# Performance work log

Hardware: AMD Instinct MI355X
Metric: run time of the kernel (lower is better)

## Reference

```python
import jax, jax.numpy as jnp
import numpy as np

B, S, D, H = 4, 2048, 1024, 16
HD = D // H
THETA = 10000.0


def _rope(x, pos, theta):
    # x: (B, H, S, HD); rotate adjacent even/odd pairs
    half = x.shape[-1] // 2
    inv_freq = theta ** (-jnp.arange(half, dtype=x.dtype) / half)  # theta^(-2k/d)
    ang = pos[:, None].astype(x.dtype) * inv_freq[None, :]         # (S, half)
    cos, sin = jnp.cos(ang), jnp.sin(ang)
    x1, x2 = x[..., 0::2], x[..., 1::2]
    o1 = x1 * cos - x2 * sin
    o2 = x1 * sin + x2 * cos
    return jnp.stack([o1, o2], axis=-1).reshape(x.shape)


def setup_inputs() -> dict:
    key = jax.random.key(0)
    ks = jax.random.split(key, 5)
    sc = 1.0 / np.sqrt(D)
    return {
        "x": jax.random.normal(ks[0], (B, S, D), jnp.float32),
        "W_Q": jax.random.normal(ks[1], (D, D), jnp.float32) * sc,
        "W_K": jax.random.normal(ks[2], (D, D), jnp.float32) * sc,
        "W_V": jax.random.normal(ks[3], (D, D), jnp.float32) * sc,
        "W_O": jax.random.normal(ks[4], (D, D), jnp.float32) * sc,
    }


def reference(x, W_Q, W_K, W_V, W_O):
    b, s, d = x.shape
    split = lambda t: t.reshape(b, s, H, HD).transpose(0, 2, 1, 3)  # (B,H,S,HD)
    q = split(x @ W_Q.T)
    k = split(x @ W_K.T)
    v = split(x @ W_V.T)
    pos = jnp.arange(s)
    q = _rope(q, pos, THETA)
    k = _rope(k, pos, THETA)
    scale = 1.0 / jnp.sqrt(jnp.asarray(HD, x.dtype))
    scores = jnp.einsum("bhqd,bhkd->bhqk", q, k) * scale
    causal = jnp.tril(jnp.ones((s, s), dtype=bool))
    scores = jnp.where(causal, scores, jnp.asarray(-jnp.inf, x.dtype))
    attn = jax.nn.softmax(scores, axis=-1)
    o = jnp.einsum("bhqk,bhkd->bhqd", attn, v)
    o = o.transpose(0, 2, 1, 3).reshape(b, s, d)
    return o @ W_O.T
```

## Files before the change

### kernel.cpp

```cpp
#include <hip/hip_runtime.h>
#include <hip/hip_bf16.h>
#include <stdint.h>

#define B_ 4
#define S_ 2048
#define D_ 1024
#define H_ 16

typedef __attribute__((ext_vector_type(4))) float f32x4;
typedef __attribute__((ext_vector_type(16))) float f32x16;
typedef __attribute__((ext_vector_type(8))) short short8;
typedef __attribute__((ext_vector_type(8))) unsigned short ushort8;
typedef __attribute__((ext_vector_type(4))) unsigned int u32x4;
typedef unsigned short u16;
typedef unsigned int u32;

__device__ __forceinline__ u16 f2bf(float f){
  return __builtin_bit_cast(u16, __hip_bfloat16(f));
}
__device__ __forceinline__ u32 pk2bf(float a, float b){
  return (u32)f2bf(a) | ((u32)f2bf(b) << 16);
}
__device__ __forceinline__ float rexp2(float x){
  float r; asm("v_exp_f32 %0, %1" : "=v"(r) : "v"(x)); return r;
}
__device__ __forceinline__ u32 cvtpk(float a, float b){
  u32 r; asm("v_cvt_pk_bf16_f32 %0, %1, %2" : "=v"(r) : "v"(a), "v"(b)); return r;
}
__device__ __forceinline__ f32x4 mfma16(short8 a, short8 b, f32x4 c){
  return __builtin_amdgcn_mfma_f32_16x16x32_bf16(a, b, c, 0, 0, 0);
}
__device__ __forceinline__ f32x16 mfma32(short8 a, short8 b, f32x16 c){
  return __builtin_amdgcn_mfma_f32_32x32x16_bf16(a, b, c, 0, 0, 0);
}
__device__ __forceinline__ void plswap(u32 &x, u32 &y){
  asm volatile("v_permlane32_swap_b32 %0, %1" : "+v"(x), "+v"(y));
}
__device__ __forceinline__ void gload16(const u16* g, u16* l){
  __builtin_amdgcn_global_load_lds((const __attribute__((address_space(1))) u32*)g,
                                   (__attribute__((address_space(3))) u32*)l, 16, 0, 0);
}

__global__ __launch_bounds__(256) void prep_kernel(const float* __restrict__ x,
                                                   const float* __restrict__ w0, const float* __restrict__ w1,
                                                   const float* __restrict__ w2, const float* __restrict__ w3,
                                                   u16* __restrict__ xb,
                                                   u16* __restrict__ o0, u16* __restrict__ o1,
                                                   u16* __restrict__ o2, u16* __restrict__ o3,
                                                   float2* __restrict__ tab){
  const int gid = blockIdx.x;
  if (gid < 8192){
    const int i = gid * 256 + threadIdx.x;
    float4 v = reinterpret_cast<const float4*>(x)[i];
    uint2 o; o.x = pk2bf(v.x, v.y); o.y = pk2bf(v.z, v.w);
    reinterpret_cast<uint2*>(xb)[i] = o;
  } else if (gid < 12288){
    const int g = gid - 8192;
    const int which = g >> 10;
    const float* in = (which==0) ? w0 : (which==1) ? w1 : (which==2) ? w2 : w3;
    u16* out = (which==0) ? o0 : (which==1) ? o1 : (which==2) ? o2 : o3;
    const int i = (g & 1023) * 256 + threadIdx.x;
    float4 v = reinterpret_cast<const float4*>(in)[i];
    uint2 o; o.x = pk2bf(v.x, v.y); o.y = pk2bf(v.z, v.w);
    reinterpret_cast<uint2*>(out)[i] = o;
  } else {
    const int idx = (gid - 12288) * 256 + threadIdx.x;
    const int i = idx & 31, s = idx >> 5;
    const float ang = (float)s * __builtin_exp2f((float)i * -0.41524101186092032f);
    float sn, cs;
    __sincosf(ang, &sn, &cs);
    tab[idx] = make_float2(cs, sn);
  }
}

template<int MODE>
__global__ __launch_bounds__(512) void gemm_bt(const u16* __restrict__ A,
                                               const u16* __restrict__ Bw,
                                               void* __restrict__ C,
                                               const float2* __restrict__ tab,
                                               int M, int N, int K){
  __shared__ __align__(16) u16 As[2][128*32];
  __shared__ __align__(16) u16 Bs[2][128*32];
  const int tid = threadIdx.x;
  const int lane = tid & 63, wid = tid >> 6;
  const int l16 = lane & 15, lq = lane >> 4;
  const int m0 = blockIdx.x * 128, n0 = blockIdx.y * 128;
  const int wr = (wid >> 2) * 64, wc = (wid & 3) * 32;
  const int srow = tid >> 2;
  const int scol = (tid & 3) * 8;
  const u16* Ag = A  + (size_t)(m0 + srow) * K + scol;
  const u16* Bg = Bw + (size_t)(n0 + srow) * K + scol;
  const int wb = wid * 512;
  gload16(Ag, &As[0][wb]);
  gload16(Bg, &Bs[0][wb]);
  __syncthreads();
  f32x4 acc[4][2] = {};
  int cur = 0;
  for (int k0 = 0; k0 < K; k0 += 32){
    if (k0 + 32 < K){
      gload16(Ag + k0 + 32, &As[cur^1][wb]);
      gload16(Bg + k0 + 32, &Bs[cur^1][wb]);
    }
    const u16* Ac = &As[cur][0];
    const u16* Bc = &Bs[cur][0];
    short8 af[4], bfr[2];
#pragma unroll
    for (int i=0;i<4;i++) af[i]  = *reinterpret_cast<const short8*>(Ac + (wr + i*16 + l16)*32 + lq*8);
#pragma unroll
    for (int j=0;j<2;j++) bfr[j] = *reinterpret_cast<const short8*>(Bc + (wc + j*16 + l16)*32 + lq*8);
    __builtin_amdgcn_s_setprio(1);
#pragma unroll
    for (int i=0;i<4;i++)
#pragma unroll
      for (int j=0;j<2;j++) acc[i][j] = mfma16(af[i], bfr[j], acc[i][j]);
    __builtin_amdgcn_s_setprio(0);
    __syncthreads();
    cur ^= 1;
  }
  const float QS = 0.18033688011112043f;
#pragma unroll
  for (int i=0;i<4;i++){
#pragma unroll
    for (int j=0;j<2;j++){
#pragma unroll
      for (int r=0;r<4;r++){
        const int m = m0 + wr + i*16 + lq*4 + r;
        const int n = n0 + wc + j*16 + l16;
        float v = acc[i][j][r];
        if (MODE == 2){
          reinterpret_cast<float*>(C)[(size_t)m * N + n] = v;
        } else if (MODE == 0){
          reinterpret_cast<u16*>(C)[(size_t)m * N + n] = f2bf(v);
        } else {
          const int b = m >> 11, s = m & 2047;
          const int h = n >> 6,  hd = n & 63;
          const float2 t = tab[(s << 5) + (hd >> 1)];
          const float partner = __shfl_xor(v, 1, 64);
          const float pm = (hd & 1) ? partner : -partner;
          float o = fmaf(v, t.x, pm * t.y);
          if (MODE == 1) o *= QS;
          reinterpret_cast<u16*>(C)[(((size_t)(b*H_ + h) * S_ + s) << 6) + hd] = f2bf(o);
        }
      }
    }
  }
}

__global__ __launch_bounds__(256) void vt_kernel(const u16* __restrict__ V, u16* __restrict__ Vt){
  __shared__ __align__(16) u16 t[64*80];
  const int bh = blockIdx.y, b = bh >> 4, h = bh & 15;
  const int s0 = blockIdx.x * 64;
  const int tid = threadIdx.x;
  const int r = tid >> 3, seg = tid & 7;
#pragma unroll
  for (int p=0;p<2;p++){
    const int row = r + p*32;
    ushort8 v = *reinterpret_cast<const ushort8*>(V + (size_t)(b*S_ + s0 + row)*D_ + h*64 + seg*8);
    *reinterpret_cast<ushort8*>(t + row*80 + seg*8) = v;
  }
  __syncthreads();
#pragma unroll
  for (int p=0;p<2;p++){
    const int hd = r + p*32;
    ushort8 o;
#pragma unroll
    for (int j=0;j<8;j++) o[j] = t[(seg*8+j)*80 + hd];
    *reinterpret_cast<ushort8*>(Vt + ((size_t)bh*64 + hd)*S_ + s0 + seg*8) = o;
  }
}

__global__ __launch_bounds__(512, 4) void attn_kernel(const u16* __restrict__ Q,
                                                      const u16* __restrict__ Kg,
                                                      const u16* __restrict__ Vt,
                                                      u16* __restrict__ O){
  __shared__ __align__(16) u16 KV[2][2][4096];
  const int bh = blockIdx.x;
  const int px = blockIdx.y;
  const int tid = threadIdx.x, wid = tid >> 6, lane = tid & 63;
  const int l32 = lane & 31, hh = lane >> 5;
  const u16* Qb = Q  + (size_t)bh * S_ * 64;
  const u16* Kb = Kg + (size_t)bh * S_ * 64;
  const u16* Vb = Vt + (size_t)bh * 64 * S_;
  const int b = bh >> 4, head = bh & 15;
  const short8 ones8 = {0x3F80,0x3F80,0x3F80,0x3F80,0x3F80,0x3F80,0x3F80,0x3F80};
  const f32x16 Z16 = {};

  const int Loff = tid*8;
  const int rowA = Loff >> 6;
  const int swzA = Loff ^ ((rowA & 7) << 3);
  const int vcolA = swzA & 63;
  const int rsw  = (l32 & 7) << 3;

#pragma unroll 1
  for (int half = 0; half < 2; ++half){
    const int qt = half ? px : (7 - px);
    const int q0 = qt * 256;
    const int qw0 = q0 + wid*32;
    const int qg = qw0 + l32;
    short8 qf[4];
#pragma unroll
    for (int j=0;j<4;j++)
      qf[j] = *reinterpret_cast<const short8*>(Qb + (size_t)qg*64 + j*16 + hh*8);
    f32x16 oacc0 = Z16, oacc1 = Z16, lacc = Z16;

    const int nt = 4*qt + 4;
    gload16(Kb + swzA,                     &KV[0][0][wid*512]);
    gload16(Vb + (size_t)rowA*S_ + vcolA,  &KV[0][1][wid*512]);
    __syncthreads();

#pragma unroll 1
    for (int kt = 0; kt < nt; ++kt){
      const int cur = kt & 1;
      if (kt + 1 < nt){
        const int kn = (kt + 1) * 64;
        gload16(Kb + (size_t)kn*64 + swzA,          &KV[cur^1][0][wid*512]);
        gload16(Vb + (size_t)rowA*S_ + kn + vcolA,  &KV[cur^1][1][wid*512]);
      }
      const int k0 = kt * 64;
      if (k0 <= qw0 + 31){
        const u16* Kc = &KV[cur][0][0];
        const u16* Vc = &KV[cur][1][0];
        f32x16 sc0 = Z16, sc1 = Z16;
        __builtin_amdgcn_s_setprio(1);
#pragma unroll
        for (int j=0;j<4;j++){
          short8 kf0 = *reinterpret_cast<const short8*>(Kc + l32*64      + ((j*16 + hh*8) ^ rsw));
          short8 kf1 = *reinterpret_cast<const short8*>(Kc + (32+l32)*64 + ((j*16 + hh*8) ^ rsw));
          sc0 = mfma32(kf0, qf[j], sc0);
          sc1 = mfma32(kf1, qf[j], sc1);
        }
        __builtin_amdgcn_s_setprio(0);
        if (k0 + 63 > qw0){
#pragma unroll
          for (int r=0;r<16;r++){
            const int kk = k0 + (r&3) + 8*(r>>2) + 4*hh;
            if (kk > qg)      sc0[r] = -1e30f;
            if (kk + 32 > qg) sc1[r] = -1e30f;
          }
        }
#pragma unroll
        for (int r=0;r<16;r++){
          sc0[r] = rexp2(sc0[r]);
          sc1[r] = rexp2(sc1[r]);
        }
        __builtin_amdgcn_s_setprio(1);
#pragma unroll
        for (int blk=0; blk<4; ++blk){
          const f32x16 S = (blk < 2) ? sc0 : sc1;
          const int r0 = (blk & 1) * 8;
          u32 a0 = cvtpk(S[r0+0], S[r0+1]);
          u32 a1 = cvtpk(S[r0+2], S[r0+3]);
          u32 b0 = cvtpk(S[r0+4], S[r0+5]);
          u32 b1 = cvtpk(S[r0+6], S[r0+7]);
          plswap(a0, b0);
          plswap(a1, b1);
          u32x4 t4; t4[0]=a0; t4[1]=a1; t4[2]=b0; t4[3]=b1;
          const short8 pf = __builtin_bit_cast(short8, t4);
          lacc = mfma32(ones8, pf, lacc);
          short8 vf0 = *reinterpret_cast<const short8*>(Vc + l32*64      + ((blk*16 + hh*8) ^ rsw));
          short8 vf1 = *reinterpret_cast<const short8*>(Vc + (32+l32)*64 + ((blk*16 + hh*8) ^ rsw));
          oacc0 = mfma32(vf0, pf, oacc0);
          oacc1 = mfma32(vf1, pf, oacc1);
        }
        __builtin_amdgcn_s_setprio(0);
      }
      __syncthreads();
    }
    const float linv = __builtin_amdgcn_rcpf(lacc[0]);
    u16* Orow = O + (size_t)(b*S_ + qg)*D_ + head*64;
#pragma unroll
    for (int q4=0;q4<4;q4++){
      uint2 o0, o1;
      o0.x = pk2bf(oacc0[q4*4+0]*linv, oacc0[q4*4+1]*linv);
      o0.y = pk2bf(oacc0[q4*4+2]*linv, oacc0[q4*4+3]*linv);
      o1.x = pk2bf(oacc1[q4*4+0]*linv, oacc1[q4*4+1]*linv);
      o1.y = pk2bf(oacc1[q4*4+2]*linv, oacc1[q4*4+3]*linv);
      *reinterpret_cast<uint2*>(Orow + q4*8 + hh*4)      = o0;
      *reinterpret_cast<uint2*>(Orow + 32 + q4*8 + hh*4) = o1;
    }
  }
}

extern "C" void kernel_launch(void* const* d_in, const int* in_sizes, int n_in,
                              void* d_out, int out_size, void* d_ws, size_t ws_size,
                              hipStream_t stream){
  const float* x  = (const float*)d_in[0];
  const float* Wq = (const float*)d_in[1];
  const float* Wk = (const float*)d_in[2];
  const float* Wv = (const float*)d_in[3];
  const float* Wo = (const float*)d_in[4];
  char* ws = (char*)d_ws;
  u16* xb  = (u16*)(ws);
  u16* Wqb = (u16*)(ws + (16u<<20));
  u16* Wkb = (u16*)(ws + (16u<<20) + (2u<<20));
  u16* Wvb = (u16*)(ws + (16u<<20) + (4u<<20));
  u16* Wob = (u16*)(ws + (16u<<20) + (6u<<20));
  u16* Qh  = (u16*)(ws + (24u<<20));
  u16* Kh  = (u16*)(ws + (40u<<20));
  u16* Vb  = (u16*)(ws + (56u<<20));
  u16* Vt  = (u16*)(ws + (72u<<20));
  float2* tab = (float2*)(ws + (88u<<20));
  u16* Ob  = Vb;

  prep_kernel<<<12544, 256, 0, stream>>>(x, Wq, Wk, Wv, Wo, xb, Wqb, Wkb, Wvb, Wob, tab);

  dim3 gg(64, 8);
  gemm_bt<1><<<gg, 512, 0, stream>>>(xb, Wqb, Qh, tab, 8192, 1024, 1024);
  gemm_bt<3><<<gg, 512, 0, stream>>>(xb, Wkb, Kh, tab, 8192, 1024, 1024);
  gemm_bt<0><<<gg, 512, 0, stream>>>(xb, Wvb, Vb, nullptr, 8192, 1024, 1024);

  vt_kernel<<<dim3(32,64), 256, 0, stream>>>(Vb, Vt);
  attn_kernel<<<dim3(64,4), 512, 0, stream>>>(Qh, Kh, Vt, Ob);

  gemm_bt<2><<<gg, 512, 0, stream>>>(Ob, Wob, (float*)d_out, nullptr, 8192, 1024, 1024);
}
```

Before: 177.6 us.

## Triple-buffer LDS loads in GEMM and attention with one barrier per step

Both the projection GEMM and the attention kernel move from double to triple buffering of their global-to-LDS tiles. Loads are issued two stages ahead and gated with explicit vmcnt waits, which leaves a single barrier per iteration instead of two. This is meant to hide more global load latency and cut synchronisation overhead. The cost is more shared memory per block, which could lower occupancy, most likely in attention where launch bounds ask for 4 blocks of 512 threads.

```diff
diff --git a/kernel.cpp b/kernel.cpp
--- a/kernel.cpp
+++ b/kernel.cpp
@@ -40,6 +40,8 @@
   __builtin_amdgcn_global_load_lds((const __attribute__((address_space(1))) u32*)g,
                                    (__attribute__((address_space(3))) u32*)l, 16, 0, 0);
 }
+__device__ __forceinline__ void wait_vm2(){ asm volatile("s_waitcnt vmcnt(2)" ::: "memory"); }
+__device__ __forceinline__ void wait_vm0(){ asm volatile("s_waitcnt vmcnt(0)" ::: "memory"); }
 
 __global__ __launch_bounds__(256) void prep_kernel(const float* __restrict__ x,
                                                    const float* __restrict__ w0, const float* __restrict__ w1,
@@ -79,8 +81,8 @@
                                                void* __restrict__ C,
                                                const float2* __restrict__ tab,
                                                int M, int N, int K){
-  __shared__ __align__(16) u16 As[2][128*32];
-  __shared__ __align__(16) u16 Bs[2][128*32];
+  __shared__ __align__(16) u16 As[3][128*32];
+  __shared__ __align__(16) u16 Bs[3][128*32];
   const int tid = threadIdx.x;
   const int lane = tid & 63, wid = tid >> 6;
   const int l16 = lane & 15, lq = lane >> 4;
@@ -91,18 +93,24 @@
   const u16* Ag = A  + (size_t)(m0 + srow) * K + scol;
   const u16* Bg = Bw + (size_t)(n0 + srow) * K + scol;
   const int wb = wid * 512;
-  gload16(Ag, &As[0][wb]);
-  gload16(Bg, &Bs[0][wb]);
-  __syncthreads();
+  gload16(Ag,      &As[0][wb]);
+  gload16(Bg,      &Bs[0][wb]);
+  gload16(Ag + 32, &As[1][wb]);
+  gload16(Bg + 32, &Bs[1][wb]);
   f32x4 acc[4][2] = {};
-  int cur = 0;
-  for (int k0 = 0; k0 < K; k0 += 32){
-    if (k0 + 32 < K){
-      gload16(Ag + k0 + 32, &As[cur^1][wb]);
-      gload16(Bg + k0 + 32, &Bs[cur^1][wb]);
+  const int NS = 32;
+#pragma unroll 1
+  for (int ks = 0; ks < NS; ++ks){
+    if (ks + 1 < NS) wait_vm2(); else wait_vm0();
+    __builtin_amdgcn_s_barrier();
+    __builtin_amdgcn_sched_barrier(0);
+    if (ks + 2 < NS){
+      const int nb = (ks + 2) % 3;
+      gload16(Ag + (ks+2)*32, &As[nb][wb]);
+      gload16(Bg + (ks+2)*32, &Bs[nb][wb]);
     }
-    const u16* Ac = &As[cur][0];
-    const u16* Bc = &Bs[cur][0];
+    const u16* Ac = &As[ks % 3][0];
+    const u16* Bc = &Bs[ks % 3][0];
     short8 af[4], bfr[2];
 #pragma unroll
     for (int i=0;i<4;i++) af[i]  = *reinterpret_cast<const short8*>(Ac + (wr + i*16 + l16)*32 + lq*8);
@@ -114,8 +122,6 @@
 #pragma unroll
       for (int j=0;j<2;j++) acc[i][j] = mfma16(af[i], bfr[j], acc[i][j]);
     __builtin_amdgcn_s_setprio(0);
-    __syncthreads();
-    cur ^= 1;
   }
   const float QS = 0.18033688011112043f;
 #pragma unroll
@@ -173,7 +179,7 @@
                                                       const u16* __restrict__ Kg,
                                                       const u16* __restrict__ Vt,
                                                       u16* __restrict__ O){
-  __shared__ __align__(16) u16 KV[2][2][4096];
+  __shared__ __align__(16) u16 KV[3][2][4096];
   const int bh = blockIdx.x;
   const int px = blockIdx.y;
   const int tid = threadIdx.x, wid = tid >> 6, lane = tid & 63;
@@ -204,22 +210,27 @@
     f32x16 oacc0 = Z16, oacc1 = Z16, lacc = Z16;
 
     const int nt = 4*qt + 4;
-    gload16(Kb + swzA,                     &KV[0][0][wid*512]);
-    gload16(Vb + (size_t)rowA*S_ + vcolA,  &KV[0][1][wid*512]);
-    __syncthreads();
+    __builtin_amdgcn_s_barrier();
+    gload16(Kb + swzA,                          &KV[0][0][wid*512]);
+    gload16(Vb + (size_t)rowA*S_ + vcolA,       &KV[0][1][wid*512]);
+    gload16(Kb + (size_t)64*64 + swzA,          &KV[1][0][wid*512]);
+    gload16(Vb + (size_t)rowA*S_ + 64 + vcolA,  &KV[1][1][wid*512]);
 
 #pragma unroll 1
     for (int kt = 0; kt < nt; ++kt){
-      const int cur = kt & 1;
-      if (kt + 1 < nt){
-        const int kn = (kt + 1) * 64;
-        gload16(Kb + (size_t)kn*64 + swzA,          &KV[cur^1][0][wid*512]);
-        gload16(Vb + (size_t)rowA*S_ + kn + vcolA,  &KV[cur^1][1][wid*512]);
+      if (kt + 1 < nt) wait_vm2(); else wait_vm0();
+      __builtin_amdgcn_s_barrier();
+      __builtin_amdgcn_sched_barrier(0);
+      if (kt + 2 < nt){
+        const int kn = (kt + 2) * 64;
+        const int nb = (kt + 2) % 3;
+        gload16(Kb + (size_t)kn*64 + swzA,          &KV[nb][0][wid*512]);
+        gload16(Vb + (size_t)rowA*S_ + kn + vcolA,  &KV[nb][1][wid*512]);
       }
       const int k0 = kt * 64;
       if (k0 <= qw0 + 31){
-        const u16* Kc = &KV[cur][0][0];
-        const u16* Vc = &KV[cur][1][0];
+        const u16* Kc = &KV[kt % 3][0][0];
+        const u16* Vc = &KV[kt % 3][1][0];
         f32x16 sc0 = Z16, sc1 = Z16;
         __builtin_amdgcn_s_setprio(1);
 #pragma unroll
@@ -264,7 +275,6 @@
         }
         __builtin_amdgcn_s_setprio(0);
       }
-      __syncthreads();
     }
     const float linv = __builtin_amdgcn_rcpf(lacc[0]);
     u16* Orow = O + (size_t)(b*S_ + qg)*D_ + head*64;
```

After: 185.7 us. 4.6% more time.

## Double GEMM K-tile to 64 with XOR-swizzled LDS layout

Applied to the files above, without the earlier changes.

The GEMM main loop now stages 64-wide K slices instead of 32, halving the number of iterations and barriers per tile. Each thread issues two global-to-LDS loads per matrix per stage. The LDS layout uses an XOR swizzle on the column offset to avoid bank conflicts on the 128-byte rows. The loop is fixed at 16 stages, which hardcodes K=1024, and LDS use doubles, which may reduce occupancy.

```diff
diff --git a/kernel.cpp b/kernel.cpp
--- a/kernel.cpp
+++ b/kernel.cpp
@@ -79,40 +79,57 @@
                                                void* __restrict__ C,
                                                const float2* __restrict__ tab,
                                                int M, int N, int K){
-  __shared__ __align__(16) u16 As[2][128*32];
-  __shared__ __align__(16) u16 Bs[2][128*32];
+  __shared__ __align__(16) u16 As[2][128*64];
+  __shared__ __align__(16) u16 Bs[2][128*64];
   const int tid = threadIdx.x;
   const int lane = tid & 63, wid = tid >> 6;
   const int l16 = lane & 15, lq = lane >> 4;
   const int m0 = blockIdx.x * 128, n0 = blockIdx.y * 128;
   const int wr = (wid >> 2) * 64, wc = (wid & 3) * 32;
-  const int srow = tid >> 2;
-  const int scol = (tid & 3) * 8;
-  const u16* Ag = A  + (size_t)(m0 + srow) * K + scol;
-  const u16* Bg = Bw + (size_t)(n0 + srow) * K + scol;
+  const int row_s = tid >> 3;
+  const int csw = ((tid & 7) * 8) ^ ((row_s & 7) << 3);
+  const u16* Ag0 = A  + (size_t)(m0 + row_s     ) * K + csw;
+  const u16* Ag1 = A  + (size_t)(m0 + 64 + row_s) * K + csw;
+  const u16* Bg0 = Bw + (size_t)(n0 + row_s     ) * K + csw;
+  const u16* Bg1 = Bw + (size_t)(n0 + 64 + row_s) * K + csw;
   const int wb = wid * 512;
-  gload16(Ag, &As[0][wb]);
-  gload16(Bg, &Bs[0][wb]);
+  const int rsw = (l16 & 7) << 3;
+  gload16(Ag0, &As[0][wb]);
+  gload16(Ag1, &As[0][4096 + wb]);
+  gload16(Bg0, &Bs[0][wb]);
+  gload16(Bg1, &Bs[0][4096 + wb]);
   __syncthreads();
   f32x4 acc[4][2] = {};
   int cur = 0;
-  for (int k0 = 0; k0 < K; k0 += 32){
-    if (k0 + 32 < K){
-      gload16(Ag + k0 + 32, &As[cur^1][wb]);
-      gload16(Bg + k0 + 32, &Bs[cur^1][wb]);
+  const int NS = 16;
+#pragma unroll 1
+  for (int ks = 0; ks < NS; ++ks){
+    if (ks + 1 < NS){
+      const int kn = (ks + 1) * 64;
+      gload16(Ag0 + kn, &As[cur^1][wb]);
+      gload16(Ag1 + kn, &As[cur^1][4096 + wb]);
+      gload16(Bg0 + kn, &Bs[cur^1][wb]);
+      gload16(Bg1 + kn, &Bs[cur^1][4096 + wb]);
     }
     const u16* Ac = &As[cur][0];
     const u16* Bc = &Bs[cur][0];
-    short8 af[4], bfr[2];
-#pragma unroll
-    for (int i=0;i<4;i++) af[i]  = *reinterpret_cast<const short8*>(Ac + (wr + i*16 + l16)*32 + lq*8);
-#pragma unroll
-    for (int j=0;j<2;j++) bfr[j] = *reinterpret_cast<const short8*>(Bc + (wc + j*16 + l16)*32 + lq*8);
+    short8 af[2][4], bfr[2][2];
+#pragma unroll
+    for (int ks2=0;ks2<2;ks2++){
+#pragma unroll
+      for (int i=0;i<4;i++)
+        af[ks2][i] = *reinterpret_cast<const short8*>(Ac + (wr + i*16 + l16)*64 + ((ks2*32 + lq*8) ^ rsw));
+#pragma unroll
+      for (int j=0;j<2;j++)
+        bfr[ks2][j] = *reinterpret_cast<const short8*>(Bc + (wc + j*16 + l16)*64 + ((ks2*32 + lq*8) ^ rsw));
+    }
     __builtin_amdgcn_s_setprio(1);
 #pragma unroll
-    for (int i=0;i<4;i++)
-#pragma unroll
-      for (int j=0;j<2;j++) acc[i][j] = mfma16(af[i], bfr[j], acc[i][j]);
+    for (int ks2=0;ks2<2;ks2++)
+#pragma unroll
+      for (int i=0;i<4;i++)
+#pragma unroll
+        for (int j=0;j<2;j++) acc[i][j] = mfma16(af[ks2][i], bfr[ks2][j], acc[i][j]);
     __builtin_amdgcn_s_setprio(0);
     __syncthreads();
     cur ^= 1;
```

Result: faster. 163.5 us (-7.9%).
